# Optimization experiments

Measured on AMD Instinct MI355X. Metric: run time of the kernel, lower is better.

The kernel has to match this reference:

```python
import jax, jax.numpy as jnp
import numpy as np

NUM_HEADS = 8
EMBED_DIM = 512
EXPAND = 3
RPE_DIM = 512
RPE_LAYERS = 3
B, N = 4, 2048
D1 = (EXPAND * EMBED_DIM) // NUM_HEADS * NUM_HEADS  # 1536
HEAD_DIM = D1 // NUM_HEADS  # 192


def srms(x):
    # SimpleRMSNorm: x / (||x||_2 * d^{-1/2} + eps)
    d = x.shape[-1]
    rms = jnp.linalg.norm(x, axis=-1, keepdims=True) * (d ** -0.5)
    return x / (rms + 1e-8)


def rpe_net(idx, Wp, bp, Wl, bl, Wr, br):
    # idx: (m, 1) relative positions -> (m, h*head_dim)
    h = idx @ Wp.T + bp
    for i in range(Wl.shape[0]):  # fixed small layer count
        h = jax.nn.relu(srms(h)) @ Wl[i].T + bl[i]
    return jax.nn.relu(srms(h)) @ Wr.T + br


def setup_inputs() -> dict:
    key = jax.random.key(0)
    ks = jax.random.split(key, 12)
    s = 0.02
    return {
        "x": jax.random.normal(ks[0], (B, N, EMBED_DIM), jnp.float32),
        "Wu": jax.random.normal(ks[1], (D1, EMBED_DIM), jnp.float32) * s,
        "bu": jnp.zeros((D1,), jnp.float32),
        "Wv": jax.random.normal(ks[2], (D1, EMBED_DIM), jnp.float32) * s,
        "bv": jnp.zeros((D1,), jnp.float32),
        "Wo": jax.random.normal(ks[3], (EMBED_DIM, D1), jnp.float32) * s,
        "bo": jnp.zeros((EMBED_DIM,), jnp.float32),
        "Wp": jax.random.normal(ks[4], (RPE_DIM, 1), jnp.float32) * s,
        "bp": jax.random.normal(ks[5], (RPE_DIM,), jnp.float32) * s,
        "Wl": jax.random.normal(ks[6], (RPE_LAYERS, RPE_DIM, RPE_DIM), jnp.float32) * s,
        "bl": jax.random.normal(ks[7], (RPE_LAYERS, RPE_DIM), jnp.float32) * s,
        "Wr": jax.random.normal(ks[8], (NUM_HEADS * HEAD_DIM, RPE_DIM), jnp.float32) * s,
        "br": jax.random.normal(ks[9], (NUM_HEADS * HEAD_DIM,), jnp.float32) * s,
    }


def reference(x, Wu, bu, Wv, bv, Wo, bo, Wp, bp, Wl, bl, Wr, br):
    b, n, e = x.shape
    d1 = Wu.shape[0]
    hd = d1 // NUM_HEADS
    u = jax.nn.silu(x @ Wu.T + bu)                       # (b, n, d1)
    v = jax.nn.silu(x @ Wv.T + bv)                       # (b, n, d1)
    v = v.reshape(b, n, NUM_HEADS, hd).transpose(0, 2, 1, 3)  # (b, h, n, d)
    # Tno non-causal, par_type=1: indices [0, 1..n-1, 0, -(n-1)..-1]
    pos = jnp.arange(1, n, dtype=x.dtype)
    zero = jnp.zeros((1,), x.dtype)
    idx = jnp.concatenate([zero, pos, zero, -pos[::-1]])[:, None]  # (2n, 1)
    a = rpe_net(idx, Wp, bp, Wl, bl, Wr, br)             # (2n, h*d)
    a = a.reshape(2 * n, NUM_HEADS, hd).transpose(1, 0, 2)  # (h, 2n, d)
    m = 2 * n
    # circular conv of length 2n along sequence, truncate to n
    y = jnp.fft.rfft(v, m, axis=2) * jnp.fft.rfft(a, m, axis=1)[None]
    out = jnp.fft.irfft(y, m, axis=2)[:, :, :n, :]       # (b, h, n, d)
    out = out.transpose(0, 2, 1, 3).reshape(b, n, d1)    # (b, n, d1)
    return (u * out) @ Wo.T + bo
```

## Files before the change

kernel.cpp:

```cpp
#include <hip/hip_runtime.h>

#define N_SEQ 2048
#define M_FFT 4096
#define D1    1536
#define NH    8
#define HD    192
#define ED    512

typedef __bf16 bf16;
typedef __bf16 bf16x4 __attribute__((ext_vector_type(4)));
typedef __bf16 bf16x8 __attribute__((ext_vector_type(8)));
typedef float  floatx4 __attribute__((ext_vector_type(4)));
typedef float  cx __attribute__((ext_vector_type(2)));

enum { MODE_PLAIN = 0, MODE_SILU_UV = 1, MODE_AT = 3, MODE_RPE = 4 };

__device__ __forceinline__ void gload16(const void* g, void* l) {
    __builtin_amdgcn_global_load_lds(
        (const __attribute__((address_space(1))) void*)g,
        (__attribute__((address_space(3))) void*)l, 16, 0, 0);
}

template<int MODE, typename OutT>
__global__ __launch_bounds__(256) void gemm_bf16(
    const bf16* __restrict__ A, const bf16* __restrict__ Bw,
    const float* __restrict__ bias, const float* __restrict__ bias2,
    OutT* __restrict__ C, OutT* __restrict__ C2,
    int M, int Nc, int K,
    const float* __restrict__ scale_in, float* __restrict__ sumsq_out)
{
    __shared__ __align__(16) bf16 As[2][128 * 32];
    __shared__ __align__(16) bf16 Bs[2][128 * 32];

    const int tid  = threadIdx.x;
    const int row0 = blockIdx.y * 128;
    const int col0 = blockIdx.x * 128;
    const int wid  = tid >> 6;
    const int lane = tid & 63;
    const int lm   = lane & 15;
    const int lk   = lane >> 4;
    const int wm   = wid >> 1;
    const int wn   = wid & 1;
    const int ldrow  = tid >> 2;
    const int ldcol8 = (tid & 3) * 8;

    floatx4 acc[4][4] = {};

    const bf16* Ag = A  + ((size_t)(row0 + ldrow)) * K + ldcol8;
    const bf16* Bg = Bw + ((size_t)(col0 + ldrow)) * K + ldcol8;
    const int woff = (wid * 16) * 32;

    auto stage = [&](int k0, int buf) {
        gload16(Ag + k0, &As[buf][woff]);
        gload16(Ag + (size_t)64 * K + k0, &As[buf][woff + 64 * 32]);
        gload16(Bg + k0, &Bs[buf][woff]);
        gload16(Bg + (size_t)64 * K + k0, &Bs[buf][woff + 64 * 32]);
    };
    auto compute = [&](int buf) {
        bf16x8 af[4], bfr[4];
        #pragma unroll
        for (int mi = 0; mi < 4; ++mi)
            af[mi] = *(const bf16x8*)&As[buf][(wm * 64 + mi * 16 + lm) * 32 + lk * 8];
        #pragma unroll
        for (int nj = 0; nj < 4; ++nj)
            bfr[nj] = *(const bf16x8*)&Bs[buf][(wn * 64 + nj * 16 + lm) * 32 + lk * 8];
        #pragma unroll
        for (int mi = 0; mi < 4; ++mi)
            #pragma unroll
            for (int nj = 0; nj < 4; ++nj)
                acc[mi][nj] = __builtin_amdgcn_mfma_f32_16x16x32_bf16(
                    af[mi], bfr[nj], acc[mi][nj], 0, 0, 0);
    };

    const int nt = K >> 5;
    stage(0, 0);
    __syncthreads();
    for (int t = 0; t < nt; t += 2) {
        stage((t + 1) << 5, 1);
        compute(0);
        __syncthreads();
        if (t + 2 < nt) stage((t + 2) << 5, 0);
        compute(1);
        __syncthreads();
    }

    const float* bs = bias;
    OutT* dst = C;
    int cadj = 0;
    if (MODE == MODE_SILU_UV && col0 >= D1) { bs = bias2; dst = C2; cadj = D1; }

    float bcol[4];
    #pragma unroll
    for (int nj = 0; nj < 4; ++nj)
        bcol[nj] = bs[col0 - cadj + wn * 64 + nj * 16 + lm];

    if (MODE == MODE_RPE) {
        #pragma unroll
        for (int mi = 0; mi < 4; ++mi) {
            #pragma unroll
            for (int r = 0; r < 4; ++r) {
                const int row = row0 + wm * 64 + mi * 16 + lk * 4 + r;
                float sc = 1.0f;
                if (scale_in)
                    sc = 1.0f / (sqrtf(scale_in[row]) * 0.04419417382415922f + 1e-8f);
                float ssq = 0.0f;
                #pragma unroll
                for (int nj = 0; nj < 4; ++nj) {
                    const int col = col0 + wn * 64 + nj * 16 + lm;
                    float val = acc[mi][nj][r] * sc + bcol[nj];
                    ssq += val * val;
                    ((bf16*)C)[(size_t)row * Nc + col] = (bf16)fmaxf(val, 0.0f);
                }
                ssq += __shfl_xor(ssq, 1, 64);
                ssq += __shfl_xor(ssq, 2, 64);
                ssq += __shfl_xor(ssq, 4, 64);
                ssq += __shfl_xor(ssq, 8, 64);
                if (lm == 0) atomicAdd(&sumsq_out[row], ssq);
            }
        }
        return;
    }

    #pragma unroll
    for (int mi = 0; mi < 4; ++mi) {
        const int rbase = row0 + wm * 64 + mi * 16 + lk * 4;
        float sc[4];
        #pragma unroll
        for (int r = 0; r < 4; ++r) {
            sc[r] = 1.0f;
            if (MODE == MODE_AT && scale_in)
                sc[r] = 1.0f / (sqrtf(scale_in[rbase + r]) * 0.04419417382415922f + 1e-8f);
        }
        #pragma unroll
        for (int nj = 0; nj < 4; ++nj) {
            const int col = col0 - cadj + wn * 64 + nj * 16 + lm;
            float vals[4];
            #pragma unroll
            for (int r = 0; r < 4; ++r) {
                float val = acc[mi][nj][r] * sc[r] + bcol[nj];
                if (MODE == MODE_SILU_UV)
                    val = val / (1.0f + __expf(-val));
                vals[r] = val;
            }
            if (MODE == MODE_SILU_UV) {
                int b = rbase >> 11, s = rbase & 2047;
                bf16x4 o;
                #pragma unroll
                for (int r = 0; r < 4; ++r) o[r] = (bf16)vals[r];
                *(bf16x4*)&((bf16*)dst)[((size_t)(b * D1 + col)) * N_SEQ + s] = o;
            } else if (MODE == MODE_AT) {
                float4 o = make_float4(vals[0], vals[1], vals[2], vals[3]);
                *(float4*)&((float*)C)[(size_t)col * M + rbase] = o;
            } else {
                #pragma unroll
                for (int r = 0; r < 4; ++r)
                    C[(size_t)(rbase + r) * Nc + col] = (OutT)vals[r];
            }
        }
    }
}

__global__ __launch_bounds__(256) void f2b_all_kernel(
    const float* __restrict__ x,  const float* __restrict__ s0,
    const float* __restrict__ s1, const float* __restrict__ s2,
    const float* __restrict__ s3, const float* __restrict__ s4,
    const float* __restrict__ Wp, const float* __restrict__ bp,
    bf16* __restrict__ x_bf, bf16* __restrict__ w_bf,
    float* __restrict__ sumsq, bf16* __restrict__ g0,
    float* __restrict__ twd)
{
    const int bid = blockIdx.x;
    const int tid = threadIdx.x;
    __shared__ float red[4];

    if (bid < 7936) {
        const float* src;
        bf16* dst;
        size_t off;
        if (bid < 4096) {
            src = x; dst = x_bf; off = (size_t)bid * 1024;
        } else {
            int t = bid - 4096;
            int seg = t / 768;
            src = seg == 0 ? s0 : seg == 1 ? s1 : seg == 2 ? s2
                : seg == 3 ? s3 : s4;
            dst = w_bf + (size_t)seg * 786432;
            off = (size_t)(t % 768) * 1024;
        }
        size_t i = off + (size_t)tid * 4;
        float4 f = *(const float4*)(src + i);
        union { bf16 h[4]; short4 s; } u4;
        u4.h[0] = (bf16)f.x; u4.h[1] = (bf16)f.y;
        u4.h[2] = (bf16)f.z; u4.h[3] = (bf16)f.w;
        *(short4*)(dst + i) = u4.s;
    } else if (bid < 7948) {
        size_t i = (size_t)(bid - 7936) * 1024 + (size_t)tid * 4;
        *(float4*)(sumsq + i) = make_float4(0.f, 0.f, 0.f, 0.f);
    } else if (bid < 12044) {
        const int j = bid - 7948;
        float idxv = (j < N_SEQ) ? (float)j
                                 : (j == N_SEQ ? 0.0f : (float)(j - 2 * N_SEQ));
        float h1 = idxv * Wp[tid] + bp[tid];
        float h2 = idxv * Wp[tid + 256] + bp[tid + 256];
        float ss = h1 * h1 + h2 * h2;
        #pragma unroll
        for (int off = 32; off > 0; off >>= 1) ss += __shfl_down(ss, off, 64);
        if ((tid & 63) == 0) red[tid >> 6] = ss;
        __syncthreads();
        float tot = red[0] + red[1] + red[2] + red[3];
        float scale = 1.0f / (sqrtf(tot) * 0.04419417382415922f + 1e-8f);
        g0[(size_t)j * ED + tid]       = (bf16)fmaxf(h1 * scale, 0.0f);
        g0[(size_t)j * ED + tid + 256] = (bf16)fmaxf(h2 * scale, 0.0f);
    } else {
        const int idx = (bid - 12044) * 256 + tid;
        const int j = idx >> 4, tau = idx & 15;
        float sA, cA;
        __sincosf(-6.283185307179586f * (float)(j * tau) * (1.0f / 4096.0f),
                  &sA, &cA);
        cx w; w.x = cA; w.y = sA;
        ((cx*)twd)[idx] = w;
    }
}

#define FFT_LDS_SZ 4381

__device__ __forceinline__ int fpad(int i) { return i + (i >> 4) + 2 * (i >> 8); }

__device__ __forceinline__ cx mkcx(float a, float b) { cx r; r.x = a; r.y = b; return r; }
__device__ __forceinline__ cx cmul(cx a, cx b) {
    cx br = mkcx(-b.y, b.x);
    return a.xx * b + a.yy * br;
}
__device__ __forceinline__ cx cmul_cj(cx a, cx b) {
    cx bc = mkcx(b.x, -b.y);
    cx br = mkcx(b.y, b.x);
    return a.xx * bc + a.yy * br;
}
__device__ __forceinline__ cx cneg_i(cx a) { return mkcx(a.y, -a.x); }
__device__ __forceinline__ cx cpos_i(cx a) { return mkcx(-a.y, a.x); }
__host__ __device__ constexpr int brev4(int t) {
    return ((t & 1) << 3) | ((t & 2) << 1) | ((t & 4) >> 1) | ((t & 8) >> 3);
}

#define CC1 0.9238795325112867f
#define SS1 0.3826834323650898f
#define RR2 0.7071067811865476f

template<bool HZ>
__device__ __forceinline__ void fft16_dif_r4(cx x[16]) {
    const cx W1 = mkcx( CC1, -SS1);
    const cx W2 = mkcx( RR2, -RR2);
    const cx W3 = mkcx( SS1, -CC1);
    const cx W6 = mkcx(-RR2, -RR2);
    const cx W9 = mkcx(-CC1,  SS1);
    #pragma unroll
    for (int n = 0; n < 4; ++n) {
        cx A, B, C, D;
        if (HZ) { A = x[n]; C = x[n]; B = x[n + 4]; D = x[n + 4]; }
        else {
            A = x[n] + x[n + 8];      C = x[n] - x[n + 8];
            B = x[n + 4] + x[n + 12]; D = x[n + 4] - x[n + 12];
        }
        cx s = A - B;
        cx nid = cneg_i(D);
        cx m = C + nid;
        cx p = C - nid;
        x[n] = A + B;
        if (n == 0)      { x[4] = s;            x[8]  = m;           x[12] = p; }
        else if (n == 1) { x[5] = cmul(s, W2);  x[9]  = cmul(m, W1); x[13] = cmul(p, W3); }
        else if (n == 2) { x[6] = cneg_i(s);    x[10] = cmul(m, W2); x[14] = cmul(p, W6); }
        else             { x[7] = cmul(s, W6);  x[11] = cmul(m, W3); x[15] = cmul(p, W9); }
    }
    #pragma unroll
    for (int q = 0; q < 16; q += 4) {
        cx a = x[q], b = x[q + 1], c = x[q + 2], d = x[q + 3];
        cx a1 = a + c, c1 = a - c;
        cx b1 = b + d, d1 = cneg_i(b - d);
        x[q]     = a1 + b1;
        x[q + 1] = a1 - b1;
        x[q + 2] = c1 + d1;
        x[q + 3] = c1 - d1;
    }
}

template<bool HALF_OUT>
__device__ __forceinline__ void fft16_dit_inv_r4(cx x[16]) {
    const cx V1 = mkcx( CC1, SS1);
    const cx V2 = mkcx( RR2, RR2);
    const cx V3 = mkcx( SS1, CC1);
    const cx V6 = mkcx(-RR2, RR2);
    #pragma unroll
    for (int q = 0; q < 16; q += 4) {
        cx a = x[q], b = x[q + 1], c = x[q + 2], d = x[q + 3];
        cx a1 = a + b, b1 = a - b;
        cx c1 = c + d, d1 = c - d;
        cx t = cpos_i(d1);
        x[q]     = a1 + c1;
        x[q + 2] = a1 - c1;
        x[q + 1] = b1 + t;
        x[q + 3] = b1 - t;
    }
    #pragma unroll
    for (int n = 0; n < 4; ++n) {
        cx t1, t2;
        if (n == 0)      { t1 = x[4];             t2 = x[12]; }
        else if (n == 1) { t1 = cmul(x[5],  V2);  t2 = cmul(x[13], V2); }
        else if (n == 2) { t1 = cpos_i(x[6]);     t2 = cpos_i(x[14]); }
        else             { t1 = cmul(x[7],  V6);  t2 = cmul(x[15], V6); }
        cx P = x[n] + t1, Q = x[n] - t1;
        cx R = x[n + 8] + t2, S = x[n + 8] - t2;
        cx t, u;
        if (n == 0)      { t = R;            u = S; }
        else if (n == 1) { t = cmul(R, V1);  u = cmul(S, V1); }
        else if (n == 2) { t = cmul(R, V2);  u = cmul(S, V2); }
        else             { t = cmul(R, V3);  u = cmul(S, V3); }
        cx iu = cpos_i(u);
        x[n]     = P + t;
        x[n + 4] = Q + iu;
        if (!HALF_OUT) {
            x[n + 8]  = P - t;
            x[n + 12] = Q - iu;
        }
    }
}

template<bool CONJ>
__device__ __forceinline__ void apply_tw(cx v[16], const cx tw[16]) {
    #pragma unroll
    for (int tau = 1; tau < 16; ++tau) {
        const int q = brev4(tau);
        v[q] = CONJ ? cmul_cj(v[q], tw[tau]) : cmul(v[q], tw[tau]);
    }
}

template<bool CONJ>
__device__ __forceinline__ void apply_tw_lds(cx v[16], const cx* twrow) {
    #pragma unroll
    for (int tau = 1; tau < 16; ++tau) {
        cx w = twrow[tau * 16];
        const int q = brev4(tau);
        v[q] = CONJ ? cmul_cj(v[q], w) : cmul(v[q], w);
    }
}

template<bool HALF_ZERO>
__device__ __forceinline__ void fft4096_fwd_core(
    cx* d, int tid, const cx tw[16], const cx* tw2lds, cx v[16])
{
    {
        fft16_dif_r4<HALF_ZERO>(v);
        apply_tw<false>(v, tw);
        cx* base = d + fpad(tid);
        #pragma unroll
        for (int p = 0; p < 16; ++p) base[274 * p] = v[p];
    }
    __syncthreads();
    {
        cx* base = d + fpad(((tid >> 4) << 8) + (tid & 15));
        #pragma unroll
        for (int t = 0; t < 16; ++t) v[t] = base[17 * t];
        fft16_dif_r4<false>(v);
        apply_tw_lds<false>(v, tw2lds + (tid & 15));
        #pragma unroll
        for (int p = 0; p < 16; ++p) base[17 * p] = v[p];
    }
    __syncthreads();
    {
        cx* base = d + fpad(tid << 4);
        #pragma unroll
        for (int t = 0; t < 16; ++t) v[t] = base[t];
        fft16_dif_r4<false>(v);
        #pragma unroll
        for (int p = 0; p < 16; ++p) base[p] = v[p];
    }
    __syncthreads();
}

__global__ __launch_bounds__(256, 4) void fft_a_kernel(
    const float* a_t, cx* __restrict__ A0s, cx* A1s,
    const cx* __restrict__ Twd)
{
    __shared__ cx data[FFT_LDS_SZ];
    __shared__ cx tw2lds[256];
    const int tid = threadIdx.x;
    const int r = blockIdx.x;

    cx tw[16];
    {
        const cx* Tr1 = Twd + (tid << 4);
        #pragma unroll
        for (int t = 1; t < 16; ++t) tw[t] = Tr1[t];
        tw2lds[(tid >> 4) * 16 + (tid & 15)] = Twd[(tid & 15) * 256 + (tid >> 4)];
    }

    const float* r0 = a_t + (size_t)(2 * r) * M_FFT;
    const float* r1 = r0 + M_FFT;
    cx v[16];
    #pragma unroll
    for (int t = 0; t < 16; ++t)
        v[t] = mkcx(r0[tid + 256 * t], r1[tid + 256 * t]);

    fft4096_fwd_core<false>(data, tid, tw, tw2lds, v);

    const float c = 0.25f / 4096.0f;
    cx* A0row = A0s + (size_t)r * 4096;
    cx* A1row = A1s + (size_t)r * 4096;
    if (tid == 0) {
        #pragma unroll
        for (int i = 0; i < 16; ++i) {
            const int p2 = (i < 2) ? i : (i ^ ((1 << (31 - __clz(i))) - 1));
            cx Wk = data[fpad(i)];
            cx Wm = data[fpad(p2)];
            cx cjWm = mkcx(Wm.x, -Wm.y);
            A0row[i] = c * (Wk + cjWm);
            A1row[i] = c * cneg_i(Wk - cjWm);
        }
    } else {
        const int base = tid << 4;
        const int mask = (1 << (31 - __clz(base))) - 1;
        const cx* zb  = data + fpad(base);
        const cx* zb2 = data + fpad((base ^ mask) - 15);
        #pragma unroll
        for (int i = 0; i < 16; ++i) {
            cx Wk = zb[i];
            cx Wm = zb2[15 - i];
            cx cjWm = mkcx(Wm.x, -Wm.y);
            A0row[base + i] = c * (Wk + cjWm);
            A1row[base + i] = c * cneg_i(Wk - cjWm);
        }
    }
}

__global__ __launch_bounds__(256, 4) void fft_conv_kernel(
    const bf16* __restrict__ v_t, const cx* __restrict__ A0s,
    const cx* __restrict__ A1s, const bf16* __restrict__ u_t,
    bf16* __restrict__ gated_t, const cx* __restrict__ Twd)
{
    __shared__ cx data[FFT_LDS_SZ];
    __shared__ cx tw2lds[256];
    const int tid = threadIdx.x;
    const int bx = blockIdx.x;
    const int xcd  = bx & 7;
    const int slot = bx >> 3;
    const int b    = slot & 3;
    const int r    = (slot >> 2) * 8 + xcd;
    const int ch = 2 * r;

    cx tw[16];
    {
        const cx* Tr1 = Twd + (tid << 4);
        #pragma unroll
        for (int t = 1; t < 16; ++t) tw[t] = Tr1[t];
        tw2lds[(tid >> 4) * 16 + (tid & 15)] = Twd[(tid & 15) * 256 + (tid >> 4)];
    }

    const bf16* z0 = v_t + ((size_t)(b * D1 + ch)) * N_SEQ;
    const bf16* z1 = z0 + N_SEQ;
    cx v[16];
    #pragma unroll
    for (int t = 0; t < 8; ++t)
        v[t] = mkcx((float)z0[tid + 256 * t], (float)z1[tid + 256 * t]);

    fft4096_fwd_core<true>(data, tid, tw, tw2lds, v);

    const cx* A0row = A0s + (size_t)r * 4096;
    const cx* A1row = A1s + (size_t)r * 4096;
    const int pbase = tid << 4;
    {
        float4 a0pf[8], a1pf[8];
        {
            const float4* A0p = (const float4*)(A0row + pbase);
            const float4* A1p = (const float4*)(A1row + pbase);
            #pragma unroll
            for (int i = 0; i < 8; ++i) { a0pf[i] = A0p[i]; a1pf[i] = A1p[i]; }
        }
        auto pf = [](const float4* p, int i) -> cx {
            return (i & 1) ? mkcx(p[i >> 1].z, p[i >> 1].w)
                           : mkcx(p[i >> 1].x, p[i >> 1].y);
        };
        if (tid == 0) {
            #pragma unroll
            for (int i = 0; i < 16; ++i) {
                const int p2 = (i < 2) ? i : (i ^ ((1 << (31 - __clz(i))) - 1));
                cx Zk = data[fpad(i)];
                cx Zm = data[fpad(p2)];
                cx cjZm = mkcx(Zm.x, -Zm.y);
                cx V0 = Zk + cjZm;
                cx V1 = cneg_i(Zk - cjZm);
                v[i] = cmul(V0, pf(a0pf, i)) + cpos_i(cmul(V1, pf(a1pf, i)));
            }
        } else {
            const int mask = (1 << (31 - __clz(pbase))) - 1;
            const cx* zb  = data + fpad(pbase);
            const cx* zb2 = data + fpad((pbase ^ mask) - 15);
            #pragma unroll
            for (int i = 0; i < 16; ++i) {
                cx Zk = zb[i];
                cx Zm = zb2[15 - i];
                cx cjZm = mkcx(Zm.x, -Zm.y);
                cx V0 = Zk + cjZm;
                cx V1 = cneg_i(Zk - cjZm);
                v[i] = cmul(V0, pf(a0pf, i)) + cpos_i(cmul(V1, pf(a1pf, i)));
            }
        }
        __syncthreads();
        fft16_dit_inv_r4<false>(v);
        cx* base = data + fpad(pbase);
        #pragma unroll
        for (int i = 0; i < 16; ++i) base[i] = v[i];
    }
    __syncthreads();
    {
        cx* base = data + fpad(((tid >> 4) << 8) + (tid & 15));
        #pragma unroll
        for (int p = 0; p < 16; ++p) v[p] = base[17 * p];
        apply_tw_lds<true>(v, tw2lds + (tid & 15));
        fft16_dit_inv_r4<false>(v);
        #pragma unroll
        for (int t = 0; t < 16; ++t) base[17 * t] = v[t];
    }
    __syncthreads();
    {
        cx* base = data + fpad(tid);
        #pragma unroll
        for (int p = 0; p < 16; ++p) v[p] = base[274 * p];
        apply_tw<true>(v, tw);
        fft16_dit_inv_r4<true>(v);
        #pragma unroll
        for (int t = 0; t < 8; ++t) base[274 * t] = v[t];
    }
    __syncthreads();

    const bf16* u0 = u_t + ((size_t)(b * D1 + ch)) * N_SEQ;
    const bf16* u1 = u0 + N_SEQ;
    bf16* g0 = gated_t + ((size_t)(b * D1 + ch)) * N_SEQ;
    bf16* g1 = g0 + N_SEQ;
    {
        const int t = tid * 8;
        const cx* base = data + fpad(t);
        bf16x8 ua = *(const bf16x8*)(u0 + t);
        bf16x8 ub = *(const bf16x8*)(u1 + t);
        bf16x8 oa, ob;
        #pragma unroll
        for (int i = 0; i < 8; ++i) {
            cx y = base[i];
            oa[i] = (bf16)(y.x * (float)ua[i]);
            ob[i] = (bf16)(y.y * (float)ub[i]);
        }
        *(bf16x8*)(g0 + t) = oa;
        *(bf16x8*)(g1 + t) = ob;
    }
}

__global__ __launch_bounds__(256) void transpose_cs_kernel(
    const bf16* __restrict__ in, bf16* __restrict__ outp)
{
    __shared__ bf16 tile[64 * 68];
    const int c0 = blockIdx.x * 64;
    const int m0 = blockIdx.y * 64;
    const int b  = m0 >> 11;
    const int s0 = m0 & 2047;
    const int tid = threadIdx.x;
    const int cl = tid >> 4;
    const int sc = (tid & 15) * 4;
    #pragma unroll
    for (int p = 0; p < 4; ++p) {
        int c = p * 16 + cl;
        bf16x4 v = *(const bf16x4*)&in[((size_t)(b * D1 + c0 + c)) * N_SEQ + s0 + sc];
        *(bf16x4*)&tile[c * 68 + sc] = v;
    }
    __syncthreads();
    const int sl = tid >> 4;
    const int cc = (tid & 15) * 4;
    #pragma unroll
    for (int p = 0; p < 4; ++p) {
        int s = p * 16 + sl;
        bf16x4 o;
        #pragma unroll
        for (int j = 0; j < 4; ++j) o[j] = tile[(cc + j) * 68 + s];
        *(bf16x4*)&outp[((size_t)(m0 + s)) * D1 + c0 + cc] = o;
    }
}

extern "C" void kernel_launch(void* const* d_in, const int* in_sizes, int n_in,
                              void* d_out, int out_size, void* d_ws, size_t ws_size,
                              hipStream_t stream)
{
    const float* x  = (const float*)d_in[0];
    const float* Wu = (const float*)d_in[1];
    const float* bu = (const float*)d_in[2];
    const float* Wv = (const float*)d_in[3];
    const float* bv = (const float*)d_in[4];
    const float* Wo = (const float*)d_in[5];
    const float* bo = (const float*)d_in[6];
    const float* Wp = (const float*)d_in[7];
    const float* bp = (const float*)d_in[8];
    const float* Wl = (const float*)d_in[9];
    const float* bl = (const float*)d_in[10];
    const float* Wr = (const float*)d_in[11];
    const float* br = (const float*)d_in[12];
    float* out = (float*)d_out;

    float* ws      = (float*)d_ws;
    float* a_t     = ws;
    float* A0spec  = a_t   + 6291456;
    float* sumsq   = A0spec + 6291456;
    float* twd     = sumsq + 12288;
    bf16*  bfws    = (bf16*)(twd + 8192);
    bf16*  x_bf    = bfws;
    bf16*  w_bf    = x_bf    + 4194304;
    bf16*  Wuv_bf  = w_bf;
    bf16*  Wo_bf   = w_bf    + 2 * 786432;
    bf16*  Wl_bf   = Wo_bf   + 786432;
    bf16*  Wr_bf   = Wl_bf   + 786432;
    bf16*  gA      = Wr_bf   + 786432;
    bf16*  gB      = gA      + 2097152;
    bf16*  u_t     = gB      + 2097152;
    bf16*  v_t     = u_t     + 12582912;
    bf16*  gated_t = v_t     + 12582912;
    bf16*  gated   = gated_t + 12582912;

    dim3 blk(256);

    f2b_all_kernel<<<4096 + 5 * 768 + 12 + 4096 + 16, blk, 0, stream>>>(
        x, Wu, Wv, Wo, Wl, Wr, Wp, bp, x_bf, w_bf, sumsq, gA, twd);

    gemm_bf16<MODE_SILU_UV, bf16><<<dim3(24, 64), blk, 0, stream>>>(
        x_bf, Wuv_bf, bu, bv, u_t, v_t, 8192, 2 * D1, ED, nullptr, nullptr);

    bf16* gin = gA;
    bf16* gout = gB;
    for (int i = 0; i < 3; ++i) {
        const float* sin_p = (i == 0) ? nullptr : sumsq + (size_t)(i - 1) * 4096;
        gemm_bf16<MODE_RPE, bf16><<<dim3(4, 32), blk, 0, stream>>>(
            gin, Wl_bf + (size_t)i * ED * ED, bl + (size_t)i * ED, nullptr,
            gout, nullptr, 4096, ED, ED, sin_p, sumsq + (size_t)i * 4096);
        bf16* t = gin; gin = gout; gout = t;
    }
    gemm_bf16<MODE_AT, float><<<dim3(12, 32), blk, 0, stream>>>(
        gin, Wr_bf, br, nullptr, a_t, nullptr, 4096, D1, ED,
        sumsq + 2 * 4096, nullptr);

    fft_a_kernel<<<768, blk, 0, stream>>>(
        a_t, (cx*)A0spec, (cx*)a_t, (const cx*)twd);
    fft_conv_kernel<<<3072, blk, 0, stream>>>(
        v_t, (const cx*)A0spec, (const cx*)a_t, u_t, gated_t, (const cx*)twd);

    transpose_cs_kernel<<<dim3(24, 128), blk, 0, stream>>>(gated_t, gated);

    gemm_bf16<MODE_PLAIN, float><<<dim3(4, 64), blk, 0, stream>>>(
        gated, Wo_bf, bo, nullptr, out, nullptr, 8192, ED, D1,
        nullptr, nullptr);
}
```

Before: 357.2 us.

## Process two batches per FFT conv block to share spectra and barriers

Each fft_conv block now runs two batch elements for the same channel pair, using two LDS buffers. The A spectrum loads, twiddle setup and barriers are shared across both FFTs, and the independent work interleaves between barriers. The aim is to cut redundant global spectrum loads and sync overhead and raise ILP. In exchange it doubles LDS per block, lowers launch bounds occupancy from 4 to 2 and halves the grid, which could hurt latency hiding.

```diff
diff --git a/kernel.cpp b/kernel.cpp
--- a/kernel.cpp
+++ b/kernel.cpp
@@ -343,6 +343,102 @@
     }
 }
 
+__device__ __forceinline__ void fwd_s1_store_hz(
+    const cx vin[8], const cx tw[16], cx* d, int tid)
+{
+    cx x[16];
+    #pragma unroll
+    for (int t = 0; t < 8; ++t) x[t] = vin[t];
+    fft16_dif_r4<true>(x);
+    apply_tw<false>(x, tw);
+    cx* base = d + fpad(tid);
+    #pragma unroll
+    for (int p = 0; p < 16; ++p) base[274 * p] = x[p];
+}
+
+__device__ __forceinline__ void fwd_s2(cx* d, int tid, const cx* tw2lds)
+{
+    cx v[16];
+    cx* base = d + fpad(((tid >> 4) << 8) + (tid & 15));
+    #pragma unroll
+    for (int t = 0; t < 16; ++t) v[t] = base[17 * t];
+    fft16_dif_r4<false>(v);
+    apply_tw_lds<false>(v, tw2lds + (tid & 15));
+    #pragma unroll
+    for (int p = 0; p < 16; ++p) base[17 * p] = v[p];
+}
+
+__device__ __forceinline__ void fwd_s3(cx* d, int tid)
+{
+    cx v[16];
+    cx* base = d + fpad(tid << 4);
+    #pragma unroll
+    for (int t = 0; t < 16; ++t) v[t] = base[t];
+    fft16_dif_r4<false>(v);
+    #pragma unroll
+    for (int p = 0; p < 16; ++p) base[p] = v[p];
+}
+
+__device__ __forceinline__ void inv_s2(cx* d, int tid, const cx* tw2lds)
+{
+    cx v[16];
+    cx* base = d + fpad(((tid >> 4) << 8) + (tid & 15));
+    #pragma unroll
+    for (int p = 0; p < 16; ++p) v[p] = base[17 * p];
+    apply_tw_lds<true>(v, tw2lds + (tid & 15));
+    fft16_dit_inv_r4<false>(v);
+    #pragma unroll
+    for (int t = 0; t < 16; ++t) base[17 * t] = v[t];
+}
+
+__device__ __forceinline__ void inv_s3_half(cx* d, int tid, const cx tw[16])
+{
+    cx v[16];
+    cx* base = d + fpad(tid);
+    #pragma unroll
+    for (int p = 0; p < 16; ++p) v[p] = base[274 * p];
+    apply_tw<true>(v, tw);
+    fft16_dit_inv_r4<true>(v);
+    #pragma unroll
+    for (int t = 0; t < 8; ++t) base[274 * t] = v[t];
+}
+
+__device__ __forceinline__ void pointwise_read(
+    const cx* d, int tid, const float4 a0pf[8], const float4 a1pf[8],
+    cx v[16])
+{
+    auto pf = [](const float4* p, int i) -> cx {
+        return (i & 1) ? mkcx(p[i >> 1].z, p[i >> 1].w)
+                       : mkcx(p[i >> 1].x, p[i >> 1].y);
+    };
+    const int pbase = tid << 4;
+    if (tid == 0) {
+        #pragma unroll
+        for (int i = 0; i < 16; ++i) {
+            const int p2 = (i < 2) ? i : (i ^ ((1 << (31 - __clz(i))) - 1));
+            cx Zk = d[fpad(i)];
+            cx Zm = d[fpad(p2)];
+            cx cjZm = mkcx(Zm.x, -Zm.y);
+            cx V0 = Zk + cjZm;
+            cx V1 = cneg_i(Zk - cjZm);
+            v[i] = cmul(V0, pf(a0pf, i)) + cpos_i(cmul(V1, pf(a1pf, i)));
+        }
+    } else {
+        const int mask = (1 << (31 - __clz(pbase))) - 1;
+        const cx* zb  = d + fpad(pbase);
+        const cx* zb2 = d + fpad((pbase ^ mask) - 15);
+        #pragma unroll
+        for (int i = 0; i < 16; ++i) {
+            cx Zk = zb[i];
+            cx Zm = zb2[15 - i];
+            cx cjZm = mkcx(Zm.x, -Zm.y);
+            cx V0 = Zk + cjZm;
+            cx V1 = cneg_i(Zk - cjZm);
+            v[i] = cmul(V0, pf(a0pf, i)) + cpos_i(cmul(V1, pf(a1pf, i)));
+        }
+    }
+}
+
 template<bool HALF_ZERO>
 __device__ __forceinline__ void fft4096_fwd_core(
     cx* d, int tid, const cx tw[16], const cx* tw2lds, cx v[16])
@@ -355,24 +451,9 @@
         for (int p = 0; p < 16; ++p) base[274 * p] = v[p];
     }
     __syncthreads();
-    {
-        cx* base = d + fpad(((tid >> 4) << 8) + (tid & 15));
-        #pragma unroll
-        for (int t = 0; t < 16; ++t) v[t] = base[17 * t];
-        fft16_dif_r4<false>(v);
-        apply_tw_lds<false>(v, tw2lds + (tid & 15));
-        #pragma unroll
-        for (int p = 0; p < 16; ++p) base[17 * p] = v[p];
-    }
-    __syncthreads();
-    {
-        cx* base = d + fpad(tid << 4);
-        #pragma unroll
-        for (int t = 0; t < 16; ++t) v[t] = base[t];
-        fft16_dif_r4<false>(v);
-        #pragma unroll
-        for (int p = 0; p < 16; ++p) base[p] = v[p];
-    }
+    fwd_s2(d, tid, tw2lds);
+    __syncthreads();
+    fwd_s3(d, tid);
     __syncthreads();
 }
 
@@ -431,20 +512,22 @@
     }
 }
 
-__global__ __launch_bounds__(256, 4) void fft_conv_kernel(
+__global__ __launch_bounds__(256, 2) void fft_conv_kernel(
     const bf16* __restrict__ v_t, const cx* __restrict__ A0s,
     const cx* __restrict__ A1s, const bf16* __restrict__ u_t,
     bf16* __restrict__ gated_t, const cx* __restrict__ Twd)
 {
-    __shared__ cx data[FFT_LDS_SZ];
+    __shared__ cx data[2][FFT_LDS_SZ];
     __shared__ cx tw2lds[256];
     const int tid = threadIdx.x;
     const int bx = blockIdx.x;
     const int xcd  = bx & 7;
     const int slot = bx >> 3;
-    const int b    = slot & 3;
-    const int r    = (slot >> 2) * 8 + xcd;
-    const int ch = 2 * r;
+    const int bp   = slot & 1;
+    const int r    = (slot >> 1) * 8 + xcd;
+    const int ch   = 2 * r;
+    const int b0   = 2 * bp;
+    const int b1   = 2 * bp + 1;
 
     cx tw[16];
     {
@@ -454,101 +537,94 @@
         tw2lds[(tid >> 4) * 16 + (tid & 15)] = Twd[(tid & 15) * 256 + (tid >> 4)];
     }
 
-    const bf16* z0 = v_t + ((size_t)(b * D1 + ch)) * N_SEQ;
-    const bf16* z1 = z0 + N_SEQ;
-    cx v[16];
-    #pragma unroll
-    for (int t = 0; t < 8; ++t)
-        v[t] = mkcx((float)z0[tid + 256 * t], (float)z1[tid + 256 * t]);
-
-    fft4096_fwd_core<true>(data, tid, tw, tw2lds, v);
-
-    const cx* A0row = A0s + (size_t)r * 4096;
-    const cx* A1row = A1s + (size_t)r * 4096;
+    const bf16* z00 = v_t + ((size_t)(b0 * D1 + ch)) * N_SEQ;
+    const bf16* z01 = z00 + N_SEQ;
+    const bf16* z10 = v_t + ((size_t)(b1 * D1 + ch)) * N_SEQ;
+    const bf16* z11 = z10 + N_SEQ;
+    {
+        cx w0[8], w1[8];
+        #pragma unroll
+        for (int t = 0; t < 8; ++t)
+            w0[t] = mkcx((float)z00[tid + 256 * t], (float)z01[tid + 256 * t]);
+        #pragma unroll
+        for (int t = 0; t < 8; ++t)
+            w1[t] = mkcx((float)z10[tid + 256 * t], (float)z11[tid + 256 * t]);
+        fwd_s1_store_hz(w0, tw, data[0], tid);
+        fwd_s1_store_hz(w1, tw, data[1], tid);
+    }
+    __syncthreads();
+
+    fwd_s2(data[0], tid, tw2lds);
+    fwd_s2(data[1], tid, tw2lds);
+    __syncthreads();
+
     const int pbase = tid << 4;
+    float4 a0pf[8], a1pf[8];
     {
-        float4 a0pf[8], a1pf[8];
-        {
-            const float4* A0p = (const float4*)(A0row + pbase);
-            const float4* A1p = (const float4*)(A1row + pbase);
-            #pragma unroll
-            for (int i = 0; i < 8; ++i) { a0pf[i] = A0p[i]; a1pf[i] = A1p[i]; }
-        }
-        auto pf = [](const float4* p, int i) -> cx {
-            return (i & 1) ? mkcx(p[i >> 1].z, p[i >> 1].w)
-                           : mkcx(p[i >> 1].x, p[i >> 1].y);
-        };
-        if (tid == 0) {
-            #pragma unroll
-            for (int i = 0; i < 16; ++i) {
-                const int p2 = (i < 2) ? i : (i ^ ((1 << (31 - __clz(i))) - 1));
-                cx Zk = data[fpad(i)];
-                cx Zm = data[fpad(p2)];
-                cx cjZm = mkcx(Zm.x, -Zm.y);
-                cx V0 = Zk + cjZm;
-                cx V1 = cneg_i(Zk - cjZm);
-                v[i] = cmul(V0, pf(a0pf, i)) + cpos_i(cmul(V1, pf(a1pf, i)));
-            }
-        } else {
-            const int mask = (1 << (31 - __clz(pbase))) - 1;
-            const cx* zb  = data + fpad(pbase);
-            const cx* zb2 = data + fpad((pbase ^ mask) - 15);
-            #pragma unroll
-            for (int i = 0; i < 16; ++i) {
-                cx Zk = zb[i];
-                cx Zm = zb2[15 - i];
-                cx cjZm = mkcx(Zm.x, -Zm.y);
-                cx V0 = Zk + cjZm;
-                cx V1 = cneg_i(Zk - cjZm);
-                v[i] = cmul(V0, pf(a0pf, i)) + cpos_i(cmul(V1, pf(a1pf, i)));
-            }
-        }
-        __syncthreads();
-        fft16_dit_inv_r4<false>(v);
-        cx* base = data + fpad(pbase);
-        #pragma unroll
-        for (int i = 0; i < 16; ++i) base[i] = v[i];
-    }
-    __syncthreads();
+        const float4* A0p = (const float4*)(A0s + (size_t)r * 4096 + pbase);
+        const float4* A1p = (const float4*)(A1s + (size_t)r * 4096 + pbase);
+        #pragma unroll
+        for (int i = 0; i < 8; ++i) { a0pf[i] = A0p[i]; a1pf[i] = A1p[i]; }
+    }
+    fwd_s3(data[0], tid);
+    fwd_s3(data[1], tid);
+    __syncthreads();
+
+    cx vA[16], vB[16];
+    pointwise_read(data[0], tid, a0pf, a1pf, vA);
+    pointwise_read(data[1], tid, a0pf, a1pf, vB);
+    __syncthreads();
+    fft16_dit_inv_r4<false>(vA);
+    fft16_dit_inv_r4<false>(vB);
     {
-        cx* base = data + fpad(((tid >> 4) << 8) + (tid & 15));
-        #pragma unroll
-        for (int p = 0; p < 16; ++p) v[p] = base[17 * p];
-        apply_tw_lds<true>(v, tw2lds + (tid & 15));
-        fft16_dit_inv_r4<false>(v);
-        #pragma unroll
-        for (int t = 0; t < 16; ++t) base[17 * t] = v[t];
-    }
-    __syncthreads();
-    {
-        cx* base = data + fpad(tid);
-        #pragma unroll
-        for (int p = 0; p < 16; ++p) v[p] = base[274 * p];
-        apply_tw<true>(v, tw);
-        fft16_dit_inv_r4<true>(v);
-        #pragma unroll
-        for (int t = 0; t < 8; ++t) base[274 * t] = v[t];
-    }
-    __syncthreads();
-
-    const bf16* u0 = u_t + ((size_t)(b * D1 + ch)) * N_SEQ;
-    const bf16* u1 = u0 + N_SEQ;
-    bf16* g0 = gated_t + ((size_t)(b * D1 + ch)) * N_SEQ;
-    bf16* g1 = g0 + N_SEQ;
+        cx* baseA = data[0] + fpad(pbase);
+        cx* baseB = data[1] + fpad(pbase);
+        #pragma unroll
+        for (int i = 0; i < 16; ++i) baseA[i] = vA[i];
+        #pragma unroll
+        for (int i = 0; i < 16; ++i) baseB[i] = vB[i];
+    }
+    __syncthreads();
+
+    const bf16* u00 = u_t + ((size_t)(b0 * D1 + ch)) * N_SEQ;
+    const bf16* u01 = u00 + N_SEQ;
+    const bf16* u10 = u_t + ((size_t)(b1 * D1 + ch)) * N_SEQ;
+    const bf16* u11 = u10 + N_SEQ;
+    bf16x8 ua0 = *(const bf16x8*)(u00 + tid * 8);
+    bf16x8 ub0 = *(const bf16x8*)(u01 + tid * 8);
+    bf16x8 ua1 = *(const bf16x8*)(u10 + tid * 8);
+    bf16x8 ub1 = *(const bf16x8*)(u11 + tid * 8);
+
+    inv_s2(data[0], tid, tw2lds);
+    inv_s2(data[1], tid, tw2lds);
+    __syncthreads();
+
+    inv_s3_half(data[0], tid, tw);
+    inv_s3_half(data[1], tid, tw);
+    __syncthreads();
+
     {
         const int t = tid * 8;
-        const cx* base = data + fpad(t);
-        bf16x8 ua = *(const bf16x8*)(u0 + t);
-        bf16x8 ub = *(const bf16x8*)(u1 + t);
-        bf16x8 oa, ob;
+        bf16* g00 = gated_t + ((size_t)(b0 * D1 + ch)) * N_SEQ;
+        bf16* g01 = g00 + N_SEQ;
+        bf16* g10 = gated_t + ((size_t)(b1 * D1 + ch)) * N_SEQ;
+        bf16* g11 = g10 + N_SEQ;
+        const cx* baseA = data[0] + fpad(t);
+        const cx* baseB = data[1] + fpad(t);
+        bf16x8 oa, ob, oc, od;
         #pragma unroll
         for (int i = 0; i < 8; ++i) {
-            cx y = base[i];
-            oa[i] = (bf16)(y.x * (float)ua[i]);
-            ob[i] = (bf16)(y.y * (float)ub[i]);
-        }
-        *(bf16x8*)(g0 + t) = oa;
-        *(bf16x8*)(g1 + t) = ob;
+            cx ya = baseA[i];
+            cx yb = baseB[i];
+            oa[i] = (bf16)(ya.x * (float)ua0[i]);
+            ob[i] = (bf16)(ya.y * (float)ub0[i]);
+            oc[i] = (bf16)(yb.x * (float)ua1[i]);
+            od[i] = (bf16)(yb.y * (float)ub1[i]);
+        }
+        *(bf16x8*)(g00 + t) = oa;
+        *(bf16x8*)(g01 + t) = ob;
+        *(bf16x8*)(g10 + t) = oc;
+        *(bf16x8*)(g11 + t) = od;
     }
 }
 
@@ -643,7 +719,7 @@
 
     fft_a_kernel<<<768, blk, 0, stream>>>(
         a_t, (cx*)A0spec, (cx*)a_t, (const cx*)twd);
-    fft_conv_kernel<<<3072, blk, 0, stream>>>(
+    fft_conv_kernel<<<1536, blk, 0, stream>>>(
         v_t, (const cx*)A0spec, (const cx*)a_t, u_t, gated_t, (const cx*)twd);
 
     transpose_cs_kernel<<<dim3(24, 128), blk, 0, stream>>>(gated_t, gated);
```

New measurement: 352.4 us. Within noise of the previous version (-1.3%).
